# Performance work log

Measured on AMD Instinct MI355X. Metric: run time of the kernel, lower is better.

## Reference

```python
import jax, jax.numpy as jnp
import numpy as np

B, F, BOND, NFREQ, NOUT, INIT_STD = 16384, 256, 16, 4, 1, 0.1


def setup_inputs() -> dict:
    key = jax.random.key(0)
    ks = jax.random.split(key, 10)
    x = jax.random.uniform(ks[0], (B, F), dtype=jnp.float32)
    inp = {"x": x, "frequency_min": jnp.array(1.0, dtype=jnp.float32)}
    d_in = 1 + 2 * NFREQ  # physical leg dim = 9
    n, level = F, 0
    while n > 1:
        n2 = n // 2
        d_out = NOUT if n == 2 else BOND
        # stack all same-level node tensors: [n_pairs, d_left, d_right, d_out]
        inp[f"W{level}"] = jax.random.normal(ks[level + 1], (n2, d_in, d_in, d_out), dtype=jnp.float32) * INIT_STD
        d_in, n, level = d_out, n2, level + 1
    return inp


def reference(x, frequency_min, W0, W1, W2, W3, W4, W5, W6, W7):
    Ws = [W0, W1, W2, W3, W4, W5, W6, W7]
    nfreq = (W0.shape[1] - 1) // 2
    # Fourier feature map: [B, F, 1+2*nfreq]
    xs = (x * frequency_min)[..., None]
    freqs = jnp.arange(1, nfreq + 1, dtype=x.dtype)
    feats = jnp.concatenate(
        [jnp.ones_like(xs), jnp.sin(xs * freqs), jnp.cos(xs * freqs)], axis=-1
    )
    nodes = feats  # [B, n_nodes, d]
    for W in Ws:
        left = nodes[:, 0::2]   # [B, n/2, d]
        right = nodes[:, 1::2]  # [B, n/2, d]
        # batched pairwise bilinear contraction over all nodes of one level
        nodes = jnp.einsum('bni,nijd,bnj->bnd', left, W, right)
    return nodes[:, 0, :]  # [B, NOUT]
```

## Files before the change

kernel.cpp:

```cpp
#include <hip/hip_runtime.h>
#include <math.h>

#define BTOT 16384

typedef __attribute__((ext_vector_type(8))) short s16x8;
typedef __attribute__((ext_vector_type(4))) float f32x4;
typedef __attribute__((ext_vector_type(4))) uint u32x4;
typedef __attribute__((ext_vector_type(2))) float f32x2;
typedef __attribute__((ext_vector_type(2))) uint u32x2;

#define OFF0 0u
#define OFF1 655360u
#define OFF2 1179648u
#define OFF3 1441792u
#define OFF4 1572864u
#define OFF5 1638400u
#define OFF6 1671168u
#define OFF7 1687552u

__device__ __forceinline__ ushort rtn_bf16(float x) {
  uint u = __builtin_bit_cast(uint, x);
  uint r = u + 0x7fffu + ((u >> 16) & 1u);
  return (ushort)(r >> 16);
}

__global__ __launch_bounds__(256) void wprep_kernel(
    const float* __restrict__ W0, const float* __restrict__ W1,
    const float* __restrict__ W2, const float* __restrict__ W3,
    const float* __restrict__ W4, const float* __restrict__ W5,
    const float* __restrict__ W6, const float* __restrict__ W7,
    ushort* __restrict__ U) {
  int blk = blockIdx.x;
  const float* Wsrc; ushort* dst; int ktN, din; bool dout1 = false;
  if (blk < 128)      { Wsrc = W0 + blk * 1296;         dst = U + OFF0 + (size_t)blk * 5120;         ktN = 5; din = 9;  }
  else if (blk < 192) { Wsrc = W1 + (blk - 128) * 4096; dst = U + OFF1 + (size_t)(blk - 128) * 8192; ktN = 8; din = 16; }
  else if (blk < 224) { Wsrc = W2 + (blk - 192) * 4096; dst = U + OFF2 + (size_t)(blk - 192) * 8192; ktN = 8; din = 16; }
  else if (blk < 240) { Wsrc = W3 + (blk - 224) * 4096; dst = U + OFF3 + (size_t)(blk - 224) * 8192; ktN = 8; din = 16; }
  else if (blk < 248) { Wsrc = W4 + (blk - 240) * 4096; dst = U + OFF4 + (size_t)(blk - 240) * 8192; ktN = 8; din = 16; }
  else if (blk < 252) { Wsrc = W5 + (blk - 248) * 4096; dst = U + OFF5 + (size_t)(blk - 248) * 8192; ktN = 8; din = 16; }
  else if (blk < 254) { Wsrc = W6 + (blk - 252) * 4096; dst = U + OFF6 + (size_t)(blk - 252) * 8192; ktN = 8; din = 16; }
  else                { Wsrc = W7;                      dst = U + OFF7;                              ktN = 8; din = 16; dout1 = true; }
  int entries = ktN * 512;
  for (int e = threadIdx.x; e < entries; e += 256) {
    int kt = e >> 9, l = (e >> 3) & 63, jv = e & 7;
    int k = kt * 32 + ((l >> 4) << 3) + jv;
    int i = k >> 4, j = k & 15, n = l & 15;
    float w;
    if (dout1) w = (n == 0) ? Wsrc[i * 16 + j] : 0.f;
    else       w = (i < din && j < din) ? Wsrc[(i * din + j) * 16 + n] : 0.f;
    uint u = __builtin_bit_cast(uint, w);
    uint h = u & 0xffff0000u;
    dst[e] = (ushort)(h >> 16);
    dst[entries + e] = rtn_bf16(w - __builtin_bit_cast(float, h));
  }
}

template <int KTN, bool L0M>
__device__ __forceinline__ f32x4 mfma_core(const float* Lcol, const float* Rcol,
                                           const int ld, const ushort* __restrict__ Wf,
                                           int lane) {
  const int g = lane >> 4;
  const int j0 = (g & 1) * 8, gh = g >> 1;
  const float* Lg = Lcol + gh * ld;
  float lf[KTN];
#pragma unroll
  for (int i = 0; i < KTN; ++i) lf[i] = Lg[2 * i * ld];
  f32x2 rf2[4];
#pragma unroll
  for (int j = 0; j < 8; ++j) {
    float v = (L0M && (j0 + j >= 9)) ? 0.f : Rcol[(j0 + j) * ld];
    rf2[j >> 1][j & 1] = v;
  }
  f32x4 acc = {0.f, 0.f, 0.f, 0.f};
  const int entries = KTN * 512;
#pragma unroll
  for (int kt = 0; kt < KTN; ++kt) {
    const f32x2 li2 = {lf[kt], lf[kt]};
    u32x4 hv, lv;
#pragma unroll
    for (int jp = 0; jp < 4; ++jp) {
      f32x2 p2 = li2 * rf2[jp];
      u32x2 u2 = __builtin_bit_cast(u32x2, p2);
      u32x2 hb = u2 & 0xffff0000u;
      f32x2 h2 = __builtin_bit_cast(f32x2, hb);
      f32x2 q2 = __builtin_elementwise_fma(li2, rf2[jp], -h2);
      u32x2 uq = __builtin_bit_cast(u32x2, q2) + 0x8000u;
      hv[jp] = __builtin_amdgcn_perm(u2.y, u2.x, 0x07060302u);
      lv[jp] = __builtin_amdgcn_perm(uq.y, uq.x, 0x07060302u);
    }
    s16x8 ahi = __builtin_bit_cast(s16x8, hv);
    s16x8 alo = __builtin_bit_cast(s16x8, lv);
    const s16x8 wh = *(const s16x8*)&Wf[(kt * 64 + lane) * 8];
    const s16x8 wl = *(const s16x8*)&Wf[entries + (kt * 64 + lane) * 8];
    acc = __builtin_amdgcn_mfma_f32_16x16x32_bf16(ahi, wh, acc, 0, 0, 0);
    acc = __builtin_amdgcn_mfma_f32_16x16x32_bf16(alo, wh, acc, 0, 0, 0);
    acc = __builtin_amdgcn_mfma_f32_16x16x32_bf16(ahi, wl, acc, 0, 0, 0);
  }
  return acc;
}

__device__ __forceinline__ void feats_col(float xv, float* Fb, int col) {
  float s1 = __sinf(xv), c1 = __cosf(xv);
  Fb[0 * 68 + col] = 1.f; Fb[1 * 68 + col] = s1; Fb[5 * 68 + col] = c1;
  float sk = s1, ck = c1;
#pragma unroll
  for (int k = 2; k <= 4; ++k) {
    float sn = s1 * ck + c1 * sk, cn = c1 * ck - s1 * sk;
    sk = sn; ck = cn;
    Fb[k * 68 + col] = sk; Fb[(4 + k) * 68 + col] = ck;
  }
}

__global__ __launch_bounds__(256) void ttn_front_kernel(
    const float* __restrict__ x, const float* __restrict__ fminp,
    const ushort* __restrict__ U, float* __restrict__ s1out) {
  __shared__ __align__(16) float xt[64 * 17];
  __shared__ __align__(16) float F0[10 * 68], F1[10 * 68];
  __shared__ __align__(16) float A0[16 * 68], B0[16 * 68];
  __shared__ __align__(16) float A1[16 * 68], B1[16 * 68];
  __shared__ __align__(16) float A2[16 * 68], B2[16 * 68];

  const int tid = threadIdx.x;
  const int lane = tid & 63, w = tid >> 6;
  const int m = lane & 15, g = lane >> 4;
  const int bl = w * 16 + m;
  const int b0 = blockIdx.x * 64;
  const int s = blockIdx.y;
  const float fmin = fminp[0];

  {
    int row = w * 16 + (lane >> 2), c4 = (lane & 3) * 4;
    float4 v = *(const float4*)&x[(size_t)(b0 + row) * 256 + s * 16 + c4];
    xt[row * 17 + c4 + 0] = v.x; xt[row * 17 + c4 + 1] = v.y;
    xt[row * 17 + c4 + 2] = v.z; xt[row * 17 + c4 + 3] = v.w;
  }
  if (lane < 32) {
    int col = w * 16 + (lane & 15);
    ((lane >> 4) ? F1 : F0)[9 * 68 + col] = 0.f;
  }

  float* outG = s1out + (size_t)(s * 16) * BTOT + b0;

  auto storeL = [&](f32x4 a, float* Out) {
#pragma unroll
    for (int r = 0; r < 4; ++r) Out[m * 68 + w * 16 + g * 4 + r] = a[r];
  };

  for (int t = 0; t < 8; ++t) {
    if (lane < 32) {
      int b_loc = lane & 15, side = lane >> 4;
      float xv = xt[(w * 16 + b_loc) * 17 + 2 * t + side] * fmin;
      feats_col(xv, side ? F1 : F0, w * 16 + b_loc);
    }
    f32x4 a = mfma_core<5, true>(&F0[bl], &F1[bl], 68,
                                 U + OFF0 + (size_t)(8 * s + t) * 5120, lane);
    storeL(a, (t & 1) ? B0 : A0);
    if (t & 1) {
      f32x4 c1 = mfma_core<8, false>(&A0[bl], &B0[bl], 68,
                                     U + OFF1 + (size_t)(4 * s + (t >> 1)) * 8192, lane);
      storeL(c1, ((t >> 1) & 1) ? B1 : A1);
      if ((t & 3) == 3) {
        f32x4 c2 = mfma_core<8, false>(&A1[bl], &B1[bl], 68,
                                       U + OFF2 + (size_t)(2 * s + (t >> 2)) * 8192, lane);
        storeL(c2, ((t >> 2) & 1) ? B2 : A2);
        if (t == 7) {
          f32x4 c3 = mfma_core<8, false>(&A2[bl], &B2[bl], 68,
                                         U + OFF3 + (size_t)s * 8192, lane);
#pragma unroll
          for (int r = 0; r < 4; ++r)
            outG[(size_t)m * BTOT + w * 16 + g * 4 + r] = c3[r];
        }
      }
    }
  }
}

__global__ __launch_bounds__(256) void backA_kernel(
    const float* __restrict__ s1, const ushort* __restrict__ U,
    float* __restrict__ s2) {
  __shared__ __align__(16) float T[4][64 * 17];
  const int tid = threadIdx.x;
  const int lane = tid & 63, w = tid >> 6;
  const int m = lane & 15, g = lane >> 4;
  const int unit = blockIdx.x * 4 + w;
  const int tile = unit >> 2, n5 = unit & 3;
  const int b0 = tile * 16;
  float* Tw = T[w];

#pragma unroll
  for (int it = 0; it < 4; ++it) {
    int flat = it * 64 + lane;
    int r = flat >> 2, c4 = (flat & 3) * 4;
    float4 v = *(const float4*)&s1[(size_t)(n5 * 64 + r) * BTOT + b0 + c4];
    Tw[r * 17 + c4 + 0] = v.x; Tw[r * 17 + c4 + 1] = v.y;
    Tw[r * 17 + c4 + 2] = v.z; Tw[r * 17 + c4 + 3] = v.w;
  }
  f32x4 a0 = mfma_core<8, false>(&Tw[m], &Tw[16 * 17 + m], 17,
                                 U + OFF4 + (size_t)(2 * n5) * 8192, lane);
#pragma unroll
  for (int r = 0; r < 4; ++r) Tw[(0 + m) * 17 + g * 4 + r] = a0[r];
  f32x4 a1 = mfma_core<8, false>(&Tw[32 * 17 + m], &Tw[48 * 17 + m], 17,
                                 U + OFF4 + (size_t)(2 * n5 + 1) * 8192, lane);
#pragma unroll
  for (int r = 0; r < 4; ++r) Tw[(32 + m) * 17 + g * 4 + r] = a1[r];
  f32x4 a2 = mfma_core<8, false>(&Tw[m], &Tw[32 * 17 + m], 17,
                                 U + OFF5 + (size_t)n5 * 8192, lane);
#pragma unroll
  for (int r = 0; r < 4; ++r)
    s2[(size_t)(n5 * 16 + m) * BTOT + b0 + g * 4 + r] = a2[r];
}

__global__ __launch_bounds__(256) void backB_kernel(
    const float* __restrict__ s2, const ushort* __restrict__ U,
    float* __restrict__ out) {
  __shared__ __align__(16) float T[4][64 * 17];
  const int tid = threadIdx.x;
  const int lane = tid & 63, w = tid >> 6;
  const int m = lane & 15, g = lane >> 4;
  const int tile = blockIdx.x * 4 + w;
  const int b0 = tile * 16;
  float* Tw = T[w];

#pragma unroll
  for (int it = 0; it < 4; ++it) {
    int flat = it * 64 + lane;
    int r = flat >> 2, c4 = (flat & 3) * 4;
    float4 v = *(const float4*)&s2[(size_t)r * BTOT + b0 + c4];
    Tw[r * 17 + c4 + 0] = v.x; Tw[r * 17 + c4 + 1] = v.y;
    Tw[r * 17 + c4 + 2] = v.z; Tw[r * 17 + c4 + 3] = v.w;
  }
  f32x4 a0 = mfma_core<8, false>(&Tw[m], &Tw[16 * 17 + m], 17, U + OFF6, lane);
#pragma unroll
  for (int r = 0; r < 4; ++r) Tw[(0 + m) * 17 + g * 4 + r] = a0[r];
  f32x4 a1 = mfma_core<8, false>(&Tw[32 * 17 + m], &Tw[48 * 17 + m], 17,
                                 U + OFF6 + 8192, lane);
#pragma unroll
  for (int r = 0; r < 4; ++r) Tw[(32 + m) * 17 + g * 4 + r] = a1[r];
  f32x4 a2 = mfma_core<8, false>(&Tw[m], &Tw[32 * 17 + m], 17, U + OFF7, lane);
  if (m == 0) {
#pragma unroll
    for (int r = 0; r < 4; ++r) out[b0 + g * 4 + r] = a2[r];
  }
}

extern "C" void kernel_launch(void* const* d_in, const int* in_sizes, int n_in,
                              void* d_out, int out_size, void* d_ws, size_t ws_size,
                              hipStream_t stream) {
  const float* x    = (const float*)d_in[0];
  const float* fmin = (const float*)d_in[1];
  const float* W0   = (const float*)d_in[2];
  const float* W1   = (const float*)d_in[3];
  const float* W2   = (const float*)d_in[4];
  const float* W3   = (const float*)d_in[5];
  const float* W4   = (const float*)d_in[6];
  const float* W5   = (const float*)d_in[7];
  const float* W6   = (const float*)d_in[8];
  const float* W7   = (const float*)d_in[9];
  float* out = (float*)d_out;

  ushort* U = (ushort*)d_ws;
  float* s1 = (float*)((char*)d_ws + (4u << 20));
  float* s2 = (float*)((char*)d_ws + (4u << 20) + (size_t)16 * 16 * BTOT * 4);

  wprep_kernel<<<255, 256, 0, stream>>>(W0, W1, W2, W3, W4, W5, W6, W7, U);
  ttn_front_kernel<<<dim3(256, 16), 256, 0, stream>>>(x, fmin, U, s1);
  backA_kernel<<<1024, 256, 0, stream>>>(s1, U, s2);
  backB_kernel<<<256, 256, 0, stream>>>(s2, U, out);
}
```

Measured before the change: 272.5 us.

## Fuse back-tree kernels into one and trim front kernel shared memory

Merges the two back-end tree kernels into a single block-per-16-samples kernel that runs levels 4 through 7 in shared memory with block barriers. This removes the s2 intermediate round trip through global memory and one kernel launch. The front kernel drops its x staging tile and reads x straight from global, changes the shared row stride to 67, adds a minimum-blocks-per-CU hint of 5, and hoists the weight loads above the bf16 split math. The fused back kernel leaves most waves idle during its last two levels.

Measured after the change: 249.7 us. -8.4%, faster.

```diff
diff --git a/kernel.cpp b/kernel.cpp
--- a/kernel.cpp
+++ b/kernel.cpp
@@ -75,6 +75,8 @@
   const int entries = KTN * 512;
 #pragma unroll
   for (int kt = 0; kt < KTN; ++kt) {
+    const s16x8 wh = *(const s16x8*)&Wf[(kt * 64 + lane) * 8];
+    const s16x8 wl = *(const s16x8*)&Wf[entries + (kt * 64 + lane) * 8];
     const f32x2 li2 = {lf[kt], lf[kt]};
     u32x4 hv, lv;
 #pragma unroll
@@ -90,8 +92,6 @@
     }
     s16x8 ahi = __builtin_bit_cast(s16x8, hv);
     s16x8 alo = __builtin_bit_cast(s16x8, lv);
-    const s16x8 wh = *(const s16x8*)&Wf[(kt * 64 + lane) * 8];
-    const s16x8 wl = *(const s16x8*)&Wf[entries + (kt * 64 + lane) * 8];
     acc = __builtin_amdgcn_mfma_f32_16x16x32_bf16(ahi, wh, acc, 0, 0, 0);
     acc = __builtin_amdgcn_mfma_f32_16x16x32_bf16(alo, wh, acc, 0, 0, 0);
     acc = __builtin_amdgcn_mfma_f32_16x16x32_bf16(ahi, wl, acc, 0, 0, 0);
@@ -99,26 +99,27 @@
   return acc;
 }
 
+#define LDF 67
+
 __device__ __forceinline__ void feats_col(float xv, float* Fb, int col) {
   float s1 = __sinf(xv), c1 = __cosf(xv);
-  Fb[0 * 68 + col] = 1.f; Fb[1 * 68 + col] = s1; Fb[5 * 68 + col] = c1;
+  Fb[0 * LDF + col] = 1.f; Fb[1 * LDF + col] = s1; Fb[5 * LDF + col] = c1;
   float sk = s1, ck = c1;
 #pragma unroll
   for (int k = 2; k <= 4; ++k) {
     float sn = s1 * ck + c1 * sk, cn = c1 * ck - s1 * sk;
     sk = sn; ck = cn;
-    Fb[k * 68 + col] = sk; Fb[(4 + k) * 68 + col] = ck;
-  }
-}
-
-__global__ __launch_bounds__(256) void ttn_front_kernel(
+    Fb[k * LDF + col] = sk; Fb[(4 + k) * LDF + col] = ck;
+  }
+}
+
+__global__ __launch_bounds__(256, 5) void ttn_front_kernel(
     const float* __restrict__ x, const float* __restrict__ fminp,
     const ushort* __restrict__ U, float* __restrict__ s1out) {
-  __shared__ __align__(16) float xt[64 * 17];
-  __shared__ __align__(16) float F0[10 * 68], F1[10 * 68];
-  __shared__ __align__(16) float A0[16 * 68], B0[16 * 68];
-  __shared__ __align__(16) float A1[16 * 68], B1[16 * 68];
-  __shared__ __align__(16) float A2[16 * 68], B2[16 * 68];
+  __shared__ float F0[10 * LDF], F1[10 * LDF];
+  __shared__ float A0[16 * LDF], B0[16 * LDF];
+  __shared__ float A1[16 * LDF], B1[16 * LDF];
+  __shared__ float A2[16 * LDF], B2[16 * LDF];
 
   const int tid = threadIdx.x;
   const int lane = tid & 63, w = tid >> 6;
@@ -128,43 +129,38 @@
   const int s = blockIdx.y;
   const float fmin = fminp[0];
 
-  {
-    int row = w * 16 + (lane >> 2), c4 = (lane & 3) * 4;
-    float4 v = *(const float4*)&x[(size_t)(b0 + row) * 256 + s * 16 + c4];
-    xt[row * 17 + c4 + 0] = v.x; xt[row * 17 + c4 + 1] = v.y;
-    xt[row * 17 + c4 + 2] = v.z; xt[row * 17 + c4 + 3] = v.w;
-  }
   if (lane < 32) {
     int col = w * 16 + (lane & 15);
-    ((lane >> 4) ? F1 : F0)[9 * 68 + col] = 0.f;
-  }
-
+    ((lane >> 4) ? F1 : F0)[9 * LDF + col] = 0.f;
+  }
+
+  const float* xw = x + (size_t)(b0 + w * 16 + (lane & 15)) * 256 + s * 16;
   float* outG = s1out + (size_t)(s * 16) * BTOT + b0;
 
   auto storeL = [&](f32x4 a, float* Out) {
 #pragma unroll
-    for (int r = 0; r < 4; ++r) Out[m * 68 + w * 16 + g * 4 + r] = a[r];
+    for (int r = 0; r < 4; ++r) Out[m * LDF + w * 16 + g * 4 + r] = a[r];
   };
 
   for (int t = 0; t < 8; ++t) {
     if (lane < 32) {
-      int b_loc = lane & 15, side = lane >> 4;
-      float xv = xt[(w * 16 + b_loc) * 17 + 2 * t + side] * fmin;
-      feats_col(xv, side ? F1 : F0, w * 16 + b_loc);
-    }
-    f32x4 a = mfma_core<5, true>(&F0[bl], &F1[bl], 68,
+      int side = lane >> 4;
+      float xv = xw[2 * t + side] * fmin;
+      feats_col(xv, side ? F1 : F0, w * 16 + (lane & 15));
+    }
+    f32x4 a = mfma_core<5, true>(&F0[bl], &F1[bl], LDF,
                                  U + OFF0 + (size_t)(8 * s + t) * 5120, lane);
     storeL(a, (t & 1) ? B0 : A0);
     if (t & 1) {
-      f32x4 c1 = mfma_core<8, false>(&A0[bl], &B0[bl], 68,
+      f32x4 c1 = mfma_core<8, false>(&A0[bl], &B0[bl], LDF,
                                      U + OFF1 + (size_t)(4 * s + (t >> 1)) * 8192, lane);
       storeL(c1, ((t >> 1) & 1) ? B1 : A1);
       if ((t & 3) == 3) {
-        f32x4 c2 = mfma_core<8, false>(&A1[bl], &B1[bl], 68,
+        f32x4 c2 = mfma_core<8, false>(&A1[bl], &B1[bl], LDF,
                                        U + OFF2 + (size_t)(2 * s + (t >> 2)) * 8192, lane);
         storeL(c2, ((t >> 2) & 1) ? B2 : A2);
         if (t == 7) {
-          f32x4 c3 = mfma_core<8, false>(&A2[bl], &B2[bl], 68,
+          f32x4 c3 = mfma_core<8, false>(&A2[bl], &B2[bl], LDF,
                                          U + OFF3 + (size_t)s * 8192, lane);
 #pragma unroll
           for (int r = 0; r < 4; ++r)
@@ -175,71 +171,55 @@
   }
 }
 
-__global__ __launch_bounds__(256) void backA_kernel(
+__global__ __launch_bounds__(256) void ttn_back_kernel(
     const float* __restrict__ s1, const ushort* __restrict__ U,
-    float* __restrict__ s2) {
-  __shared__ __align__(16) float T[4][64 * 17];
+    float* __restrict__ out) {
+  __shared__ float T[256 * 17];
   const int tid = threadIdx.x;
   const int lane = tid & 63, w = tid >> 6;
   const int m = lane & 15, g = lane >> 4;
-  const int unit = blockIdx.x * 4 + w;
-  const int tile = unit >> 2, n5 = unit & 3;
-  const int b0 = tile * 16;
-  float* Tw = T[w];
+  const int b0 = blockIdx.x * 16;
 
 #pragma unroll
   for (int it = 0; it < 4; ++it) {
-    int flat = it * 64 + lane;
-    int r = flat >> 2, c4 = (flat & 3) * 4;
-    float4 v = *(const float4*)&s1[(size_t)(n5 * 64 + r) * BTOT + b0 + c4];
-    Tw[r * 17 + c4 + 0] = v.x; Tw[r * 17 + c4 + 1] = v.y;
-    Tw[r * 17 + c4 + 2] = v.z; Tw[r * 17 + c4 + 3] = v.w;
-  }
-  f32x4 a0 = mfma_core<8, false>(&Tw[m], &Tw[16 * 17 + m], 17,
-                                 U + OFF4 + (size_t)(2 * n5) * 8192, lane);
-#pragma unroll
-  for (int r = 0; r < 4; ++r) Tw[(0 + m) * 17 + g * 4 + r] = a0[r];
-  f32x4 a1 = mfma_core<8, false>(&Tw[32 * 17 + m], &Tw[48 * 17 + m], 17,
-                                 U + OFF4 + (size_t)(2 * n5 + 1) * 8192, lane);
-#pragma unroll
-  for (int r = 0; r < 4; ++r) Tw[(32 + m) * 17 + g * 4 + r] = a1[r];
-  f32x4 a2 = mfma_core<8, false>(&Tw[m], &Tw[32 * 17 + m], 17,
-                                 U + OFF5 + (size_t)n5 * 8192, lane);
-#pragma unroll
-  for (int r = 0; r < 4; ++r)
-    s2[(size_t)(n5 * 16 + m) * BTOT + b0 + g * 4 + r] = a2[r];
-}
-
-__global__ __launch_bounds__(256) void backB_kernel(
-    const float* __restrict__ s2, const ushort* __restrict__ U,
-    float* __restrict__ out) {
-  __shared__ __align__(16) float T[4][64 * 17];
-  const int tid = threadIdx.x;
-  const int lane = tid & 63, w = tid >> 6;
-  const int m = lane & 15, g = lane >> 4;
-  const int tile = blockIdx.x * 4 + w;
-  const int b0 = tile * 16;
-  float* Tw = T[w];
-
-#pragma unroll
-  for (int it = 0; it < 4; ++it) {
-    int flat = it * 64 + lane;
-    int r = flat >> 2, c4 = (flat & 3) * 4;
-    float4 v = *(const float4*)&s2[(size_t)r * BTOT + b0 + c4];
-    Tw[r * 17 + c4 + 0] = v.x; Tw[r * 17 + c4 + 1] = v.y;
-    Tw[r * 17 + c4 + 2] = v.z; Tw[r * 17 + c4 + 3] = v.w;
-  }
-  f32x4 a0 = mfma_core<8, false>(&Tw[m], &Tw[16 * 17 + m], 17, U + OFF6, lane);
-#pragma unroll
-  for (int r = 0; r < 4; ++r) Tw[(0 + m) * 17 + g * 4 + r] = a0[r];
-  f32x4 a1 = mfma_core<8, false>(&Tw[32 * 17 + m], &Tw[48 * 17 + m], 17,
-                                 U + OFF6 + 8192, lane);
-#pragma unroll
-  for (int r = 0; r < 4; ++r) Tw[(32 + m) * 17 + g * 4 + r] = a1[r];
-  f32x4 a2 = mfma_core<8, false>(&Tw[m], &Tw[32 * 17 + m], 17, U + OFF7, lane);
-  if (m == 0) {
-#pragma unroll
-    for (int r = 0; r < 4; ++r) out[b0 + g * 4 + r] = a2[r];
+    int idx = it * 256 + tid;
+    int r = idx >> 2, c4 = (idx & 3) * 4;
+    float4 v = *(const float4*)&s1[(size_t)r * BTOT + b0 + c4];
+    T[r * 17 + c4 + 0] = v.x; T[r * 17 + c4 + 1] = v.y;
+    T[r * 17 + c4 + 2] = v.z; T[r * 17 + c4 + 3] = v.w;
+  }
+  __syncthreads();
+
+  const int q = w, base = 64 * q;
+  f32x4 a0 = mfma_core<8, false>(&T[base * 17 + m], &T[(base + 16) * 17 + m], 17,
+                                 U + OFF4 + (size_t)(2 * q) * 8192, lane);
+  f32x4 a1 = mfma_core<8, false>(&T[(base + 32) * 17 + m], &T[(base + 48) * 17 + m], 17,
+                                 U + OFF4 + (size_t)(2 * q + 1) * 8192, lane);
+#pragma unroll
+  for (int r = 0; r < 4; ++r) {
+    T[(base + m) * 17 + g * 4 + r] = a0[r];
+    T[(base + 32 + m) * 17 + g * 4 + r] = a1[r];
+  }
+  f32x4 a2 = mfma_core<8, false>(&T[base * 17 + m], &T[(base + 32) * 17 + m], 17,
+                                 U + OFF5 + (size_t)q * 8192, lane);
+#pragma unroll
+  for (int r = 0; r < 4; ++r) T[(base + m) * 17 + g * 4 + r] = a2[r];
+  __syncthreads();
+
+  if (w < 2) {
+    f32x4 a3 = mfma_core<8, false>(&T[(128 * w) * 17 + m], &T[(128 * w + 64) * 17 + m],
+                                   17, U + OFF6 + (size_t)w * 8192, lane);
+#pragma unroll
+    for (int r = 0; r < 4; ++r) T[(128 * w + m) * 17 + g * 4 + r] = a3[r];
+  }
+  __syncthreads();
+
+  if (w == 0) {
+    f32x4 a4 = mfma_core<8, false>(&T[m], &T[128 * 17 + m], 17, U + OFF7, lane);
+    if (m == 0) {
+#pragma unroll
+      for (int r = 0; r < 4; ++r) out[b0 + g * 4 + r] = a4[r];
+    }
   }
 }
 
@@ -260,10 +240,8 @@
 
   ushort* U = (ushort*)d_ws;
   float* s1 = (float*)((char*)d_ws + (4u << 20));
-  float* s2 = (float*)((char*)d_ws + (4u << 20) + (size_t)16 * 16 * BTOT * 4);
 
   wprep_kernel<<<255, 256, 0, stream>>>(W0, W1, W2, W3, W4, W5, W6, W7, U);
   ttn_front_kernel<<<dim3(256, 16), 256, 0, stream>>>(x, fmin, U, s1);
-  backA_kernel<<<1024, 256, 0, stream>>>(s1, U, s2);
-  backB_kernel<<<256, 256, 0, stream>>>(s2, U, out);
-}
+  ttn_back_kernel<<<1024, 256, 0, stream>>>(s1, U, out);
+}
```
